# Kernel optimization log

Measured on AMD Instinct MI355X. Metric: run time of the kernel, lower is better.

The kernel has to match this reference:

```python
import jax, jax.numpy as jnp
import numpy as np

TEMPERATURE = 8.0  # sqrt(d_attn) with d_attn = 64
EPS = 1e-12


def _cv_softmax(z):
    """Complex softmax: softmax applied to magnitude, phase preserved.
    result = softmax(|z|, axis=-1) * z / |z|
    """
    mag = jnp.abs(z)                          # [B,H,S,S] real
    w = jax.nn.softmax(mag, axis=-1)          # softmax over magnitudes
    phase = z / jnp.maximum(mag, EPS)         # unit-modulus phase, guarded at 0
    return (w * phase).astype(z.dtype)


def setup_inputs() -> dict:
    key = jax.random.key(0)
    ks = jax.random.split(key, 6)
    shape = (4, 8, 2048, 64)  # [B, H, S, D]
    names = ["q_real", "q_imag", "k_real", "k_imag", "v_real", "v_imag"]
    return {n: jax.random.normal(k, shape, dtype=jnp.float32) for n, k in zip(names, ks)}


def reference(q_real, q_imag, k_real, k_imag, v_real, v_imag):
    q = jax.lax.complex(q_real, q_imag)
    k = jax.lax.complex(k_real, k_imag)
    v = jax.lax.complex(v_real, v_imag)
    # attn = (Q / t) K^T   (complex matmul)   [B,H,S,S]
    attn = jnp.einsum("bhsd,bhtd->bhst", q / TEMPERATURE, k)
    attn = _cv_softmax(attn)  # dropout is identity in eval mode
    out = jnp.einsum("bhst,bhtd->bhsd", attn, v)  # [B,H,S,D] complex
    # return as stacked real array [2, B, H, S, D] (real, imag)
    return jnp.stack([jnp.real(out), jnp.imag(out)], axis=0)
```

## Files before the change

kernel.cpp:

```cpp
#include <hip/hip_runtime.h>
#include <math.h>

typedef _Float16 half8   __attribute__((ext_vector_type(8)));
typedef _Float16 half4_t __attribute__((ext_vector_type(4)));
typedef float    floatx4 __attribute__((ext_vector_type(4)));

namespace {

constexpr int S  = 2048;
constexpr int D  = 64;
constexpr int BH = 32;
constexpr int QT = 64;
constexpr int PST = 40;
constexpr float INV_T = 0.125f;
constexpr size_t PLANE = (size_t)BH * S * D;
constexpr float MBIAS = 2.772588722239781f;

#define MFMA16(a, b, c) __builtin_amdgcn_mfma_f32_16x16x32_f16((a), (b), (c), 0, 0, 0)

typedef __attribute__((address_space(1))) const unsigned int guint;
typedef __attribute__((address_space(3))) unsigned int luint;

__device__ __forceinline__ void gl_lds16(const _Float16* g, _Float16* l) {
    __builtin_amdgcn_global_load_lds((guint*)g, (luint*)l, 16, 0, 0);
}

__global__ __launch_bounds__(256)
void prep_all(const float* __restrict__ kr, const float* __restrict__ ki,
              const float* __restrict__ vr, const float* __restrict__ vi,
              _Float16* __restrict__ okr, _Float16* __restrict__ oki,
              _Float16* __restrict__ ovr, _Float16* __restrict__ ovi)
{
    __shared__ _Float16 tile[64][72];
    const int z  = (int)blockIdx.z;
    const int bh = (int)blockIdx.y, t0 = (int)blockIdx.x * 64;
    const int tid = (int)threadIdx.x;

    if (z < 2) {
        const float* src = z ? ki : kr;
        _Float16*    dst = z ? oki : okr;
        const int r = tid >> 2, cg = tid & 3;
        const size_t in = ((size_t)bh * S + t0 + r) * D + cg * 16;
        float4 f0 = *(const float4*)(src + in);
        float4 f1 = *(const float4*)(src + in + 4);
        float4 f2 = *(const float4*)(src + in + 8);
        float4 f3 = *(const float4*)(src + in + 12);
        half8 h0, h1;
        h0[0]=(_Float16)f0.x; h0[1]=(_Float16)f0.y; h0[2]=(_Float16)f0.z; h0[3]=(_Float16)f0.w;
        h0[4]=(_Float16)f1.x; h0[5]=(_Float16)f1.y; h0[6]=(_Float16)f1.z; h0[7]=(_Float16)f1.w;
        h1[0]=(_Float16)f2.x; h1[1]=(_Float16)f2.y; h1[2]=(_Float16)f2.z; h1[3]=(_Float16)f2.w;
        h1[4]=(_Float16)f3.x; h1[5]=(_Float16)f3.y; h1[6]=(_Float16)f3.z; h1[7]=(_Float16)f3.w;
        const int key = r & 7;
        const size_t ob = ((size_t)bh * S + t0 + r) * D;
        *(half8*)(dst + ob + ((cg*2    ) ^ key) * 8) = h0;
        *(half8*)(dst + ob + ((cg*2 + 1) ^ key) * 8) = h1;
    } else {
        const float* src = (z == 3) ? vi : vr;
        _Float16*    dst = (z == 3) ? ovi : ovr;
        const int r = tid & 63, cg = tid >> 6;
        const size_t in = ((size_t)bh * S + t0 + r) * D + cg * 16;
        #pragma unroll
        for (int j = 0; j < 4; ++j) {
            float4 f = *(const float4*)(src + in + j * 4);
            tile[cg*16 + j*4 + 0][r] = (_Float16)f.x;
            tile[cg*16 + j*4 + 1][r] = (_Float16)f.y;
            tile[cg*16 + j*4 + 2][r] = (_Float16)f.z;
            tile[cg*16 + j*4 + 3][r] = (_Float16)f.w;
        }
        __syncthreads();
        const int d = tid >> 2, c2 = tid & 3;
        const int key = d & 3;
        const size_t ob = ((size_t)bh * D + d) * S + t0;
        half8 a = *(const half8*)&tile[d][c2*16];
        half8 b = *(const half8*)&tile[d][c2*16 + 8];
        const int j0 = c2*2, j1 = c2*2 + 1;
        *(half8*)(dst + ob + (size_t)(((j0 & 4) | ((j0 & 3) ^ key))) * 8) = a;
        *(half8*)(dst + ob + (size_t)(((j1 & 4) | ((j1 & 3) ^ key))) * 8) = b;
    }
}

__global__ __launch_bounds__(256, 3)
void cv_attn_db(const float* __restrict__ qr_g, const float* __restrict__ qi_g,
                const _Float16* __restrict__ kh_r, const _Float16* __restrict__ kh_i,
                const _Float16* __restrict__ vt_r, const _Float16* __restrict__ vt_i,
                float* __restrict__ out)
{
    __shared__ __align__(16) _Float16 sm[2*4*2048 + 4*2*16*PST];
    _Float16* const Pb = sm + 2*4*2048;

    const int tid = (int)threadIdx.x, lane = tid & 63, wv = tid >> 6;
    const int g = lane >> 4, m = lane & 15;

    const int b   = (int)blockIdx.x;
    const int xcd = b & 7, y = b >> 3;
    const int qt  = y & 31, bh = xcd + 8 * (y >> 5);
    const int q0  = qt * QT;
    const size_t base = (size_t)bh * S * D;

    _Float16* const Pr = Pb + wv * (2*16*PST);
    _Float16* const Pi = Pr + 16*PST;

    half8 aqr[2], aqi[2], aqin[2];
    {
        const size_t qoff = base + (size_t)(q0 + wv*16 + m) * D + g*8;
        #pragma unroll
        for (int kc = 0; kc < 2; ++kc) {
            float4 r0 = *(const float4*)(qr_g + qoff + kc*32);
            float4 r1 = *(const float4*)(qr_g + qoff + kc*32 + 4);
            float4 i0 = *(const float4*)(qi_g + qoff + kc*32);
            float4 i1 = *(const float4*)(qi_g + qoff + kc*32 + 4);
            half8 hr, hi;
            hr[0]=(_Float16)(r0.x*INV_T); hr[1]=(_Float16)(r0.y*INV_T);
            hr[2]=(_Float16)(r0.z*INV_T); hr[3]=(_Float16)(r0.w*INV_T);
            hr[4]=(_Float16)(r1.x*INV_T); hr[5]=(_Float16)(r1.y*INV_T);
            hr[6]=(_Float16)(r1.z*INV_T); hr[7]=(_Float16)(r1.w*INV_T);
            hi[0]=(_Float16)(i0.x*INV_T); hi[1]=(_Float16)(i0.y*INV_T);
            hi[2]=(_Float16)(i0.z*INV_T); hi[3]=(_Float16)(i0.w*INV_T);
            hi[4]=(_Float16)(i1.x*INV_T); hi[5]=(_Float16)(i1.y*INV_T);
            hi[6]=(_Float16)(i1.z*INV_T); hi[7]=(_Float16)(i1.w*INV_T);
            aqr[kc] = hr; aqi[kc] = hi; aqin[kc] = -hi;
        }
    }

    floatx4 Or[4], Oi[4];
    float l_run[4] = {0.f, 0.f, 0.f, 0.f};
    #pragma unroll
    for (int nt = 0; nt < 4; ++nt) {
        Or[nt] = (floatx4){0.f,0.f,0.f,0.f};
        Oi[nt] = (floatx4){0.f,0.f,0.f,0.f};
    }

    auto stage = [&](int kt, _Float16* bs) {
        const int k0 = kt * 32;
        if (wv < 2) {
            const _Float16* src = (wv ? kh_i : kh_r) + ((size_t)bh*S + k0)*D + lane*8;
            _Float16* dst = bs + wv*2048;
            #pragma unroll
            for (int i = 0; i < 4; ++i)
                gl_lds16(src + i*512, dst + i*512);
        } else {
            const _Float16* src = (wv == 2 ? vt_r : vt_i)
                                + ((size_t)bh*D + (lane>>2))*S + k0 + (lane&3)*8;
            _Float16* dst = bs + wv*2048;
            #pragma unroll
            for (int i = 0; i < 4; ++i)
                gl_lds16(src + (size_t)i*16*S, dst + i*512);
        }
    };

    auto compute = [&](_Float16* bs) {
        _Float16* const Krt = bs;
        _Float16* const Kit = bs + 2048;
        _Float16* const Vrt = bs + 4096;
        _Float16* const Vit = bs + 6144;

        floatx4 Zr[2], Zi[2];
        #pragma unroll
        for (int nt = 0; nt < 2; ++nt) {
            const int rb  = (nt*16 + m) * 64;
            const int key = m & 7;
            const int ck0 = (g ^ key) * 8, ck1 = ((g + 4) ^ key) * 8;
            half8 bkr0 = *(const half8*)&Krt[rb + ck0];
            half8 bki0 = *(const half8*)&Kit[rb + ck0];
            half8 bkr1 = *(const half8*)&Krt[rb + ck1];
            half8 bki1 = *(const half8*)&Kit[rb + ck1];
            floatx4 zr = (floatx4){0.f,0.f,0.f,0.f};
            floatx4 zi = (floatx4){0.f,0.f,0.f,0.f};
            zr = MFMA16(aqr[0],  bkr0, zr);
            zr = MFMA16(aqin[0], bki0, zr);
            zr = MFMA16(aqr[1],  bkr1, zr);
            zr = MFMA16(aqin[1], bki1, zr);
            zi = MFMA16(aqr[0],  bki0, zi);
            zi = MFMA16(aqi[0],  bkr0, zi);
            zi = MFMA16(aqr[1],  bki1, zi);
            zi = MFMA16(aqi[1],  bkr1, zi);
            Zr[nt] = zr; Zi[nt] = zi;
        }

        #pragma unroll
        for (int nt = 0; nt < 2; ++nt) {
            #pragma unroll
            for (int r = 0; r < 4; ++r) {
                const float zr = Zr[nt][r], zi = Zi[nt][r];
                const float s2  = fmaf(zr, zr, fmaf(zi, zi, 1e-24f));
                const float inv = __builtin_amdgcn_rsqf(s2);
                const float mag = s2 * inv;
                const float p   = __expf(mag - MBIAS);
                l_run[r] += p;
                const float w = p * inv;
                Pr[(4*g + r)*PST + nt*16 + m] = (_Float16)(w * zr);
                Pi[(4*g + r)*PST + nt*16 + m] = (_Float16)(w * zi);
            }
        }

        half8 apr = *(const half8*)&Pr[m*PST + g*8];
        half8 api = *(const half8*)&Pi[m*PST + g*8];
        half8 nai = -api;
        #pragma unroll
        for (int nt = 0; nt < 4; ++nt) {
            const int vrb = (nt*16 + m) * 32;
            const int vck = (g ^ (m & 3)) * 8;
            half8 bvr = *(const half8*)&Vrt[vrb + vck];
            half8 bvi = *(const half8*)&Vit[vrb + vck];
            Or[nt] = MFMA16(apr, bvr, Or[nt]);
            Or[nt] = MFMA16(nai, bvi, Or[nt]);
            Oi[nt] = MFMA16(apr, bvi, Oi[nt]);
            Oi[nt] = MFMA16(api, bvr, Oi[nt]);
        }
    };

    _Float16* const buf0 = sm;
    _Float16* const buf1 = sm + 4*2048;

    stage(0, buf0);
    for (int kt = 0; kt < 64; kt += 2) {
        __syncthreads();
        stage(kt + 1, buf1);
        compute(buf0);
        __syncthreads();
        if (kt < 62) stage(kt + 2, buf0);
        compute(buf1);
    }

    #pragma unroll
    for (int off = 1; off < 16; off <<= 1)
        #pragma unroll
        for (int r = 0; r < 4; ++r)
            l_run[r] += __shfl_xor(l_run[r], off, 64);

    #pragma unroll
    for (int r = 0; r < 4; ++r) {
        const float linv = 1.0f / l_run[r];
        const size_t o = base + (size_t)(q0 + wv*16 + 4*g + r) * D + m;
        #pragma unroll
        for (int nt = 0; nt < 4; ++nt) {
            out[o + nt*16]         = Or[nt][r] * linv;
            out[PLANE + o + nt*16] = Oi[nt][r] * linv;
        }
    }
}

constexpr int ST2 = 72;
__global__ __launch_bounds__(256, 2)
void cv_attn_mfma(const float* __restrict__ qr_g, const float* __restrict__ qi_g,
                  const float* __restrict__ kr_g, const float* __restrict__ ki_g,
                  const float* __restrict__ vr_g, const float* __restrict__ vi_g,
                  float* __restrict__ out)
{
    __shared__ __align__(16) _Float16 sm[4*64*ST2 + 4*2*16*ST2];
    _Float16* const Kr = sm;
    _Float16* const Ki = Kr + 64*ST2;
    _Float16* const Vr = Ki + 64*ST2;
    _Float16* const Vi = Vr + 64*ST2;
    _Float16* const Pb = Vi + 64*ST2;

    const int tid = (int)threadIdx.x, lane = tid & 63, wv = tid >> 6;
    const int g = lane >> 4, m = lane & 15;
    const int bh = (int)blockIdx.y;
    const int q0 = (int)blockIdx.x * QT;
    const size_t base = (size_t)bh * S * D;
    _Float16* const Pr = Pb + wv * (2*16*ST2);
    _Float16* const Pi = Pr + 16*ST2;
    const int lofs = m*ST2 + g*8;

    half8 aqr[2], aqi[2], aqin[2];
    {
        const size_t qoff = base + (size_t)(q0 + wv*16 + m) * D + g*8;
        #pragma unroll
        for (int kc = 0; kc < 2; ++kc) {
            float4 r0 = *(const float4*)(qr_g + qoff + kc*32);
            float4 r1 = *(const float4*)(qr_g + qoff + kc*32 + 4);
            float4 i0 = *(const float4*)(qi_g + qoff + kc*32);
            float4 i1 = *(const float4*)(qi_g + qoff + kc*32 + 4);
            half8 hr, hi;
            hr[0]=(_Float16)(r0.x*INV_T); hr[1]=(_Float16)(r0.y*INV_T);
            hr[2]=(_Float16)(r0.z*INV_T); hr[3]=(_Float16)(r0.w*INV_T);
            hr[4]=(_Float16)(r1.x*INV_T); hr[5]=(_Float16)(r1.y*INV_T);
            hr[6]=(_Float16)(r1.z*INV_T); hr[7]=(_Float16)(r1.w*INV_T);
            hi[0]=(_Float16)(i0.x*INV_T); hi[1]=(_Float16)(i0.y*INV_T);
            hi[2]=(_Float16)(i0.z*INV_T); hi[3]=(_Float16)(i0.w*INV_T);
            hi[4]=(_Float16)(i1.x*INV_T); hi[5]=(_Float16)(i1.y*INV_T);
            hi[6]=(_Float16)(i1.z*INV_T); hi[7]=(_Float16)(i1.w*INV_T);
            aqr[kc] = hr; aqi[kc] = hi; aqin[kc] = -hi;
        }
    }

    floatx4 Or[4], Oi[4];
    float m_run[4], l_run[4];
    #pragma unroll
    for (int r = 0; r < 4; ++r) { m_run[r] = -INFINITY; l_run[r] = 0.f; }
    #pragma unroll
    for (int nt = 0; nt < 4; ++nt) {
        Or[nt] = (floatx4){0.f,0.f,0.f,0.f};
        Oi[nt] = (floatx4){0.f,0.f,0.f,0.f};
    }

    for (int kt = 0; kt < S/64; ++kt) {
        const int k0 = kt * 64;
        __syncthreads();
        if (wv < 2) {
            const float* src = (wv == 0 ? kr_g : ki_g) + base + (size_t)k0 * D;
            _Float16* dst = (wv == 0 ? Kr : Ki);
            #pragma unroll
            for (int it = 0; it < 16; ++it) {
                const int e = it*64 + lane, t = e >> 4, c4 = (e & 15) * 4;
                float4 v = *(const float4*)(src + t*64 + c4);
                half4_t hh = {(_Float16)v.x, (_Float16)v.y, (_Float16)v.z, (_Float16)v.w};
                *(half4_t*)&dst[t*ST2 + c4] = hh;
            }
        } else {
            const float* src = (wv == 2 ? vr_g : vi_g) + base + (size_t)k0 * D;
            _Float16* dst = (wv == 2 ? Vr : Vi);
            #pragma unroll
            for (int t0 = 0; t0 < 64; t0 += 4) {
                float v0 = src[(t0+0)*64 + lane];
                float v1 = src[(t0+1)*64 + lane];
                float v2 = src[(t0+2)*64 + lane];
                float v3 = src[(t0+3)*64 + lane];
                half4_t hh = {(_Float16)v0, (_Float16)v1, (_Float16)v2, (_Float16)v3};
                *(half4_t*)&dst[lane*ST2 + t0] = hh;
            }
        }
        __syncthreads();

        floatx4 Zr[4], Zi[4];
        #pragma unroll
        for (int nt = 0; nt < 4; ++nt) {
            floatx4 zr = (floatx4){0.f,0.f,0.f,0.f};
            floatx4 zi = (floatx4){0.f,0.f,0.f,0.f};
            #pragma unroll
            for (int kc = 0; kc < 2; ++kc) {
                const int o = nt*16*ST2 + lofs + kc*32;
                half8 bkr = *(const half8*)&Kr[o];
                half8 bki = *(const half8*)&Ki[o];
                zr = MFMA16(aqr[kc],  bkr, zr);
                zr = MFMA16(aqin[kc], bki, zr);
                zi = MFMA16(aqr[kc],  bki, zi);
                zi = MFMA16(aqi[kc],  bkr, zi);
            }
            Zr[nt] = zr; Zi[nt] = zi;
        }

        float mag[4][4], mt[4] = {0.f,0.f,0.f,0.f};
        #pragma unroll
        for (int nt = 0; nt < 4; ++nt)
            #pragma unroll
            for (int r = 0; r < 4; ++r) {
                const float a = Zr[nt][r], bz = Zi[nt][r];
                const float s = __builtin_amdgcn_sqrtf(a*a + bz*bz);
                mag[nt][r] = s; mt[r] = fmaxf(mt[r], s);
            }
        #pragma unroll
        for (int off = 1; off < 16; off <<= 1)
            #pragma unroll
            for (int r = 0; r < 4; ++r)
                mt[r] = fmaxf(mt[r], __shfl_xor(mt[r], off, 64));

        float alpha[4], rs[4];
        #pragma unroll
        for (int r = 0; r < 4; ++r) {
            const float mnew = fmaxf(m_run[r], mt[r]);
            alpha[r] = __expf(m_run[r] - mnew);
            m_run[r] = mnew; rs[r] = 0.f;
        }
        #pragma unroll
        for (int nt = 0; nt < 4; ++nt)
            #pragma unroll
            for (int r = 0; r < 4; ++r) {
                const float p = __expf(mag[nt][r] - m_run[r]);
                rs[r] += p;
                const float w = p * __builtin_amdgcn_rcpf(fmaxf(mag[nt][r], 1e-12f));
                Pr[(4*g + r)*ST2 + nt*16 + m] = (_Float16)(w * Zr[nt][r]);
                Pi[(4*g + r)*ST2 + nt*16 + m] = (_Float16)(w * Zi[nt][r]);
            }
        #pragma unroll
        for (int off = 1; off < 16; off <<= 1)
            #pragma unroll
            for (int r = 0; r < 4; ++r)
                rs[r] += __shfl_xor(rs[r], off, 64);
        #pragma unroll
        for (int r = 0; r < 4; ++r) l_run[r] = l_run[r]*alpha[r] + rs[r];

        #pragma unroll
        for (int nt = 0; nt < 4; ++nt)
            #pragma unroll
            for (int r = 0; r < 4; ++r) { Or[nt][r] *= alpha[r]; Oi[nt][r] *= alpha[r]; }

        half8 apr[2], api[2], apin[2];
        #pragma unroll
        for (int kc = 0; kc < 2; ++kc) {
            apr[kc]  = *(const half8*)&Pr[lofs + kc*32];
            api[kc]  = *(const half8*)&Pi[lofs + kc*32];
            apin[kc] = -api[kc];
        }
        #pragma unroll
        for (int nt = 0; nt < 4; ++nt) {
            floatx4 ors = Or[nt], ois = Oi[nt];
            #pragma unroll
            for (int kc = 0; kc < 2; ++kc) {
                const int o = nt*16*ST2 + lofs + kc*32;
                half8 bvr = *(const half8*)&Vr[o];
                half8 bvi = *(const half8*)&Vi[o];
                ors = MFMA16(apr[kc],  bvr, ors);
                ors = MFMA16(apin[kc], bvi, ors);
                ois = MFMA16(apr[kc],  bvi, ois);
                ois = MFMA16(api[kc],  bvr, ois);
            }
            Or[nt] = ors; Oi[nt] = ois;
        }
    }

    #pragma unroll
    for (int r = 0; r < 4; ++r) {
        const float linv = 1.0f / l_run[r];
        const size_t o = base + (size_t)(q0 + wv*16 + 4*g + r) * D + m;
        #pragma unroll
        for (int nt = 0; nt < 4; ++nt) {
            out[o + nt*16]         = Or[nt][r] * linv;
            out[PLANE + o + nt*16] = Oi[nt][r] * linv;
        }
    }
}

}

extern "C" void kernel_launch(void* const* d_in, const int* in_sizes, int n_in,
                              void* d_out, int out_size, void* d_ws, size_t ws_size,
                              hipStream_t stream) {
    const float* qr = (const float*)d_in[0];
    const float* qi = (const float*)d_in[1];
    const float* kr = (const float*)d_in[2];
    const float* ki = (const float*)d_in[3];
    const float* vr = (const float*)d_in[4];
    const float* vi = (const float*)d_in[5];
    float* out = (float*)d_out;

    const size_t PH = (size_t)BH * S * D;
    const size_t need = 4 * PH * sizeof(_Float16);
    if (ws_size >= need) {
        _Float16* khr = (_Float16*)d_ws;
        _Float16* khi = khr + PH;
        _Float16* vtr = khi + PH;
        _Float16* vti = vtr + PH;
        prep_all<<<dim3(32, 32, 4), 256, 0, stream>>>(kr, ki, vr, vi, khr, khi, vtr, vti);
        cv_attn_db<<<1024, 256, 0, stream>>>(qr, qi, khr, khi, vtr, vti, out);
    } else {
        cv_attn_mfma<<<dim3(32, 32), 256, 0, stream>>>(qr, qi, kr, ki, vr, vi, out);
    }
}
```

Before: 299.0 us.

## Transpose softmax probabilities in registers via permlane swaps instead of LDS

Swaps the MFMA operand order so the score tile comes out transposed, with each lane holding one query row. The probabilities are then packed to fp16 pairs and rearranged into the A-operand layout with v_permlane32/16_swap, removing the per-wave LDS scratch round trip for P. The row-sum becomes one scalar per lane, reduced across lane groups and broadcast at the end. Dropping the P scratch cuts LDS use, and the occupancy hint rises from 3 to 4 blocks, at the cost of possible register pressure.

```diff
diff --git a/kernel.cpp b/kernel.cpp
--- a/kernel.cpp
+++ b/kernel.cpp
@@ -3,7 +3,9 @@
 
 typedef _Float16 half8   __attribute__((ext_vector_type(8)));
 typedef _Float16 half4_t __attribute__((ext_vector_type(4)));
+typedef _Float16 half2_t __attribute__((ext_vector_type(2)));
 typedef float    floatx4 __attribute__((ext_vector_type(4)));
+typedef unsigned int uint4_t __attribute__((ext_vector_type(4)));
 
 namespace {
 
@@ -11,7 +13,6 @@
 constexpr int D  = 64;
 constexpr int BH = 32;
 constexpr int QT = 64;
-constexpr int PST = 40;
 constexpr float INV_T = 0.125f;
 constexpr size_t PLANE = (size_t)BH * S * D;
 constexpr float MBIAS = 2.772588722239781f;
@@ -23,6 +24,33 @@
 
 __device__ __forceinline__ void gl_lds16(const _Float16* g, _Float16* l) {
     __builtin_amdgcn_global_load_lds((guint*)g, (luint*)l, 16, 0, 0);
+}
+
+__device__ __forceinline__ unsigned pk2(float a, float b) {
+#if __has_builtin(__builtin_amdgcn_cvt_pkrtz)
+    auto h = __builtin_amdgcn_cvt_pkrtz(a, b);
+    return __builtin_bit_cast(unsigned, h);
+#else
+    half2_t h = {(_Float16)a, (_Float16)b};
+    return __builtin_bit_cast(unsigned, h);
+#endif
+}
+
+__device__ __forceinline__ void pl32swap(unsigned &a, unsigned &b) {
+    asm("v_permlane32_swap_b32 %0, %1" : "+v"(a), "+v"(b));
+}
+__device__ __forceinline__ void pl16swap(unsigned &a, unsigned &b) {
+    asm("v_permlane16_swap_b32 %0, %1" : "+v"(a), "+v"(b));
+}
+
+__device__ __forceinline__ half8 xpose4(unsigned A0, unsigned A1,
+                                        unsigned B0, unsigned B1) {
+    pl32swap(A0, B0);
+    pl32swap(A1, B1);
+    pl16swap(A0, B0);
+    pl16swap(A1, B1);
+    uint4_t d = (uint4_t){A0, A1, B0, B1};
+    return __builtin_bit_cast(half8, d);
 }
 
 __global__ __launch_bounds__(256)
@@ -79,14 +107,13 @@
     }
 }
 
-__global__ __launch_bounds__(256, 3)
+__global__ __launch_bounds__(256, 4)
 void cv_attn_db(const float* __restrict__ qr_g, const float* __restrict__ qi_g,
                 const _Float16* __restrict__ kh_r, const _Float16* __restrict__ kh_i,
                 const _Float16* __restrict__ vt_r, const _Float16* __restrict__ vt_i,
                 float* __restrict__ out)
 {
-    __shared__ __align__(16) _Float16 sm[2*4*2048 + 4*2*16*PST];
-    _Float16* const Pb = sm + 2*4*2048;
+    __shared__ __align__(16) _Float16 sm[2*4*2048];
 
     const int tid = (int)threadIdx.x, lane = tid & 63, wv = tid >> 6;
     const int g = lane >> 4, m = lane & 15;
@@ -96,9 +123,6 @@
     const int qt  = y & 31, bh = xcd + 8 * (y >> 5);
     const int q0  = qt * QT;
     const size_t base = (size_t)bh * S * D;
-
-    _Float16* const Pr = Pb + wv * (2*16*PST);
-    _Float16* const Pi = Pr + 16*PST;
 
     half8 aqr[2], aqi[2], aqin[2];
     {
@@ -123,7 +147,7 @@
     }
 
     floatx4 Or[4], Oi[4];
-    float l_run[4] = {0.f, 0.f, 0.f, 0.f};
+    float l_run = 0.f;
     #pragma unroll
     for (int nt = 0; nt < 4; ++nt) {
         Or[nt] = (floatx4){0.f,0.f,0.f,0.f};
@@ -148,11 +172,11 @@
         }
     };
 
-    auto compute = [&](_Float16* bs) {
-        _Float16* const Krt = bs;
-        _Float16* const Kit = bs + 2048;
-        _Float16* const Vrt = bs + 4096;
-        _Float16* const Vit = bs + 6144;
+    auto compute = [&](const _Float16* bs) {
+        const _Float16* const Krt = bs;
+        const _Float16* const Kit = bs + 2048;
+        const _Float16* const Vrt = bs + 4096;
+        const _Float16* const Vit = bs + 6144;
 
         floatx4 Zr[2], Zi[2];
         #pragma unroll
@@ -166,19 +190,21 @@
             half8 bki1 = *(const half8*)&Kit[rb + ck1];
             floatx4 zr = (floatx4){0.f,0.f,0.f,0.f};
             floatx4 zi = (floatx4){0.f,0.f,0.f,0.f};
-            zr = MFMA16(aqr[0],  bkr0, zr);
-            zr = MFMA16(aqin[0], bki0, zr);
-            zr = MFMA16(aqr[1],  bkr1, zr);
-            zr = MFMA16(aqin[1], bki1, zr);
-            zi = MFMA16(aqr[0],  bki0, zi);
-            zi = MFMA16(aqi[0],  bkr0, zi);
-            zi = MFMA16(aqr[1],  bki1, zi);
-            zi = MFMA16(aqi[1],  bkr1, zi);
+            zr = MFMA16(bkr0, aqr[0],  zr);
+            zr = MFMA16(bki0, aqin[0], zr);
+            zr = MFMA16(bkr1, aqr[1],  zr);
+            zr = MFMA16(bki1, aqin[1], zr);
+            zi = MFMA16(bki0, aqr[0],  zi);
+            zi = MFMA16(bkr0, aqi[0],  zi);
+            zi = MFMA16(bki1, aqr[1],  zi);
+            zi = MFMA16(bkr1, aqi[1],  zi);
             Zr[nt] = zr; Zi[nt] = zi;
         }
 
+        unsigned PkR[4], PkI[4];
         #pragma unroll
         for (int nt = 0; nt < 2; ++nt) {
+            float wr[4], wi[4];
             #pragma unroll
             for (int r = 0; r < 4; ++r) {
                 const float zr = Zr[nt][r], zi = Zi[nt][r];
@@ -186,16 +212,20 @@
                 const float inv = __builtin_amdgcn_rsqf(s2);
                 const float mag = s2 * inv;
                 const float p   = __expf(mag - MBIAS);
-                l_run[r] += p;
+                l_run += p;
                 const float w = p * inv;
-                Pr[(4*g + r)*PST + nt*16 + m] = (_Float16)(w * zr);
-                Pi[(4*g + r)*PST + nt*16 + m] = (_Float16)(w * zi);
-            }
-        }
-
-        half8 apr = *(const half8*)&Pr[m*PST + g*8];
-        half8 api = *(const half8*)&Pi[m*PST + g*8];
+                wr[r] = w * zr; wi[r] = w * zi;
+            }
+            PkR[nt*2 + 0] = pk2(wr[0], wr[1]);
+            PkR[nt*2 + 1] = pk2(wr[2], wr[3]);
+            PkI[nt*2 + 0] = pk2(wi[0], wi[1]);
+            PkI[nt*2 + 1] = pk2(wi[2], wi[3]);
+        }
+
+        half8 apr = xpose4(PkR[0], PkR[1], PkR[2], PkR[3]);
+        half8 api = xpose4(PkI[0], PkI[1], PkI[2], PkI[3]);
         half8 nai = -api;
+
         #pragma unroll
         for (int nt = 0; nt < 4; ++nt) {
             const int vrb = (nt*16 + m) * 32;
@@ -222,15 +252,12 @@
         compute(buf1);
     }
 
-    #pragma unroll
-    for (int off = 1; off < 16; off <<= 1)
-        #pragma unroll
-        for (int r = 0; r < 4; ++r)
-            l_run[r] += __shfl_xor(l_run[r], off, 64);
+    l_run += __shfl_xor(l_run, 16, 64);
+    l_run += __shfl_xor(l_run, 32, 64);
 
     #pragma unroll
     for (int r = 0; r < 4; ++r) {
-        const float linv = 1.0f / l_run[r];
+        const float linv = 1.0f / __shfl(l_run, 4*g + r, 64);
         const size_t o = base + (size_t)(q0 + wv*16 + 4*g + r) * D + m;
         #pragma unroll
         for (int nt = 0; nt < 4; ++nt) {
```

Result: faster. 283.1 us (-5.3%).
